# Kernel tuning notes

Hardware: AMD Instinct MI355X
Metric: run time of the kernel (lower is better)

Reference implementation:

```python
import jax, jax.numpy as jnp
import numpy as np

EPS = 1e-5

def _bilinear_sample(xb, ys, xs):
    # xb: [C,H,W]; ys, xs: [H,W] float sample coordinates (zero outside bounds)
    C, H, W = xb.shape
    y0 = jnp.floor(ys); x0 = jnp.floor(xs)
    y1 = y0 + 1.0;      x1 = x0 + 1.0
    wy1 = ys - y0; wy0 = 1.0 - wy1
    wx1 = xs - x0; wx0 = 1.0 - wx1
    def g(yi, xi):
        valid = (yi >= 0) & (yi < H) & (xi >= 0) & (xi < W)
        yc = jnp.clip(yi, 0, H - 1).astype(jnp.int32)
        xc = jnp.clip(xi, 0, W - 1).astype(jnp.int32)
        return xb[:, yc, xc] * valid[None].astype(xb.dtype)  # [C,H,W]
    return (g(y0, x0) * (wy0 * wx0)[None] + g(y0, x1) * (wy0 * wx1)[None]
          + g(y1, x0) * (wy1 * wx0)[None] + g(y1, x1) * (wy1 * wx1)[None])

def _deform_conv2d(x, offset, mask, w, b):
    # x:[B,C,H,W] offset:[B,18,H,W] mask:[B,9,H,W] w:[Co,C,3,3] b:[Co]
    B, C, H, W = x.shape
    Co = w.shape[0]
    ii = jnp.arange(H, dtype=x.dtype)[:, None]
    jj = jnp.arange(W, dtype=x.dtype)[None, :]
    cols = []
    for k in range(9):  # fixed 3x3 kernel positions, row-major (dy=offset[2k], dx=offset[2k+1])
        ky, kx = k // 3 - 1, k % 3 - 1
        ys = ii + ky + offset[:, 2 * k]      # [B,H,W]
        xs = jj + kx + offset[:, 2 * k + 1]
        v = jax.vmap(_bilinear_sample)(x, ys, xs)  # [B,C,H,W]
        cols.append(v * mask[:, k][:, None])
    cols = jnp.stack(cols, axis=1)               # [B,9,C,H,W]
    out = jnp.einsum('bkchw,ock->bohw', cols, w.reshape(Co, C, 9))
    return out + b[None, :, None, None]

def setup_inputs() -> dict:
    key = jax.random.key(0)
    k1, k2, k3, k4 = jax.random.split(key, 4)
    B, Cin, Cout, H, W = 8, 64, 64, 128, 128
    x = jax.random.normal(k1, (B, Cin, H, W), dtype=jnp.float32)
    # offset/mask conv: small weights so learned offsets stay O(1) pixels;
    # bias[18:]=2.0 as in the module's init (masks start near sigmoid(2))
    w_off = jax.random.normal(k2, (27, Cin, 3, 3), dtype=jnp.float32) * 0.01
    b_off = jnp.concatenate([jnp.zeros((18,), jnp.float32), jnp.full((9,), 2.0, jnp.float32)])
    w_dcn = jax.random.normal(k3, (Cout, Cin, 3, 3), dtype=jnp.float32) / np.sqrt(Cin * 9)
    b_dcn = jax.random.normal(k4, (Cout,), dtype=jnp.float32) * 0.01
    return {"x": x, "w_off": w_off, "b_off": b_off, "w_dcn": w_dcn, "b_dcn": b_dcn}

def reference(x, w_off, b_off, w_dcn, b_dcn):
    dn = ('NCHW', 'OIHW', 'NCHW')
    om = jax.lax.conv_general_dilated(x, w_off, (1, 1), 'SAME', dimension_numbers=dn)
    om = om + b_off[None, :, None, None]
    offset = om[:, :18]
    mask = jax.nn.sigmoid(om[:, 18:])
    y = _deform_conv2d(x, offset, mask, w_dcn, b_dcn)
    # InstanceNorm2d (affine=False, biased variance) + ReLU
    mu = jnp.mean(y, axis=(2, 3), keepdims=True)
    var = jnp.var(y, axis=(2, 3), keepdims=True)
    y = (y - mu) * jax.lax.rsqrt(var + EPS)
    return jax.nn.relu(y)
```

## Files before the change

### kernel.cpp

```cpp
#include <hip/hip_runtime.h>
#include <hip/hip_fp16.h>

#define BB   8
#define CIN  64
#define COUT 64
#define HH   128
#define WW   128
#define HWSZ (HH * WW)

typedef _Float16 f16x8 __attribute__((ext_vector_type(8)));
typedef _Float16 h2v   __attribute__((ext_vector_type(2)));
typedef float    f32x4 __attribute__((ext_vector_type(4)));

__device__ __forceinline__ unsigned short f2h_u(float f) {
    __half h = __float2half(f);
    return __half_as_ushort(h);
}
__device__ __forceinline__ float h2f_u(unsigned short u) {
    _Float16 f = *(_Float16*)&u;
    return (float)f;
}
__device__ __forceinline__ unsigned pk2h(float lo, float hi) {
    return (unsigned)f2h_u(lo) | ((unsigned)f2h_u(hi) << 16);
}
__device__ __forceinline__ h2v dupL(unsigned u) { h2v v = *(h2v*)&u; return (h2v){v[0], v[0]}; }
__device__ __forceinline__ h2v dupH(unsigned u) { h2v v = *(h2v*)&u; return (h2v){v[1], v[1]}; }

__device__ __forceinline__ unsigned comb2h(unsigned a, unsigned b, unsigned c, unsigned d,
                                           h2v W0, h2v W1, h2v W2, h2v W3) {
    h2v A = *(h2v*)&a, B = *(h2v*)&b, C = *(h2v*)&c, D = *(h2v*)&d;
    h2v r = A * W0;
    r += B * W1;
    r += C * W2;
    r += D * W3;
    return *(unsigned*)&r;
}


__global__ __launch_bounds__(256) void k_tr(const float* __restrict__ x,
                                            const float* __restrict__ wd,
                                            const float* __restrict__ wof,
                                            unsigned short* __restrict__ xT,
                                            unsigned short* __restrict__ wdT,
                                            unsigned short* __restrict__ wofT,
                                            float4* __restrict__ sums4)
{
    const int t = threadIdx.x;
    const int id = blockIdx.x;
    if (id >= 512) {
        if (id == 512) sums4[t] = make_float4(0.f, 0.f, 0.f, 0.f);
        int base = (id - 512) * 256 + t;
#pragma unroll
        for (int j = 0; j < 4; ++j) {
            int idx = base + j * 16384;
            if (idx < 36864) {
                int k = idx >> 12, rem = idx & 4095, co = rem >> 6, c = rem & 63;
                wdT[idx] = f2h_u(wd[(co * 64 + c) * 9 + k]);
            } else if (idx < 55296) {
                int jj = idx - 36864;
                int k = jj >> 11, rem = jj & 2047, o = rem >> 6, c = rem & 63;
                wofT[jj] = (o < 27) ? f2h_u(wof[(o * 64 + c) * 9 + k]) : 0;
            }
        }
        return;
    }
    __shared__ unsigned short tile[256 * 66];
    const int b = id & 7;
    const int p0 = (id >> 3) * 256;
#pragma unroll
    for (int i = 0; i < 16; ++i) {
        int c = i * 4 + (t >> 6);
        int pl = (t & 63) * 4;
        float4 v = *(const float4*)(x + (((size_t)b * 64 + c) << 14) + p0 + pl);
        tile[(pl + 0) * 66 + c] = f2h_u(v.x);
        tile[(pl + 1) * 66 + c] = f2h_u(v.y);
        tile[(pl + 2) * 66 + c] = f2h_u(v.z);
        tile[(pl + 3) * 66 + c] = f2h_u(v.w);
    }
    __syncthreads();
#pragma unroll
    for (int i = 0; i < 8; ++i) {
        int idd = i * 256 + t;
        int pt = idd >> 3, ck = idd & 7;
        const unsigned* srcp = (const unsigned*)&tile[pt * 66 + ck * 8];
        uint4 r;
        r.x = srcp[0]; r.y = srcp[1]; r.z = srcp[2]; r.w = srcp[3];
        *(uint4*)(xT + ((size_t)b << 20) + ((size_t)(ck >> 2) << 19)
                     + (size_t)(p0 + pt) * 32 + (ck & 3) * 8) = r;
    }
}

__global__ __launch_bounds__(256, 2) void k_off(
    const unsigned short* __restrict__ xT, const unsigned short* __restrict__ wofT,
    const float* __restrict__ bof, unsigned short* __restrict__ om)
{
    __shared__ unsigned short tile[8 * 521 * 8];
    const int t = threadIdx.x;
    const int lane = t & 63, wv = t >> 6;
    const int q = lane >> 4, l15 = lane & 15;
    const int b = blockIdx.x & 7;
    const int xblk = blockIdx.x >> 3;
    const int h0 = xblk * 2;
    const int r0 = h0 - 1;
    const unsigned short* xb = xT + ((size_t)b << 20);

#pragma unroll
    for (int i = 0; i < 17; ++i) {
        int id = i * 256 + t;
        if (id < 4160) {
            int m = id & 7, lin = id >> 3;
            int row = lin / 130, col = lin % 130;
            int gy = r0 + row, gx = col - 1;
            uint4 v = {0u, 0u, 0u, 0u};
            if (((unsigned)gy < (unsigned)HH) && ((unsigned)gx < (unsigned)WW))
                v = *(const uint4*)(xb + ((size_t)(m >> 2) << 19)
                                       + (size_t)(gy * WW + gx) * 32 + (m & 3) * 8);
            *(uint4*)&tile[(m * 521 + lin) * 8] = v;
        }
    }
    __syncthreads();

    const int hrow = h0 + (wv >> 1);
    const int c0 = (wv & 1) * 64;

    f32x4 acc[2][4];
#pragma unroll
    for (int mt = 0; mt < 2; ++mt)
#pragma unroll
        for (int nt = 0; nt < 4; ++nt) acc[mt][nt] = (f32x4){0.f, 0.f, 0.f, 0.f};

#pragma unroll
    for (int k = 0; k < 9; ++k) {
        const int ky = k / 3 - 1, kx = k % 3 - 1;
        const int trow = (hrow - h0) + ky + 1;
        const unsigned short* wk = wofT + k * 2048;
#pragma unroll
        for (int ks = 0; ks < 2; ++ks) {
            f16x8 af[2], bfr[4];
#pragma unroll
            for (int mt = 0; mt < 2; ++mt)
                af[mt] = *(const f16x8*)(wk + (mt * 16 + l15) * 64 + ks * 32 + q * 8);
#pragma unroll
            for (int nt = 0; nt < 4; ++nt) {
                int tc = c0 + nt * 16 + l15 + kx + 1;
                bfr[nt] = *(const f16x8*)&tile[((ks * 4 + q) * 521 + trow * 130 + tc) * 8];
            }
#pragma unroll
            for (int mt = 0; mt < 2; ++mt)
#pragma unroll
                for (int nt = 0; nt < 4; ++nt)
                    acc[mt][nt] = __builtin_amdgcn_mfma_f32_16x16x32_f16(
                        af[mt], bfr[nt], acc[mt][nt], 0, 0, 0);
        }
    }

    const int p0 = xblk * 256 + wv * 64;
    unsigned short* omb = om + (size_t)b * 27 * HWSZ;
#pragma unroll
    for (int mt = 0; mt < 2; ++mt)
#pragma unroll
        for (int r = 0; r < 4; ++r) {
            int o = mt * 16 + q * 4 + r;
            if (o < 27) {
                float bias = bof[o];
#pragma unroll
                for (int nt = 0; nt < 4; ++nt) {
                    int pp = p0 + nt * 16 + l15;
                    float v = acc[mt][nt][r] + bias;
                    if (o >= 18) v = 1.f / (1.f + __expf(-v));
                    omb[(size_t)o * HWSZ + pp] = f2h_u(v);
                }
            }
        }
}

__global__ __launch_bounds__(512, 2) void k_dcn(
    const unsigned short* __restrict__ xT, const unsigned short* __restrict__ om,
    const unsigned short* __restrict__ wdT, const float* __restrict__ bd,
    unsigned short* __restrict__ yh, float2* __restrict__ sums)
{
    __shared__ unsigned short tile_sh[8 * 128 * 32];
    __shared__ uint4          meta_sh[8][64];

    const int t = threadIdx.x;
    const int lane = t & 63, wv = t >> 6;
    const int q = lane >> 4, l15 = lane & 15;
    const int b = blockIdx.x & 7;
    const int pblk = (blockIdx.x >> 3) * 512;
    const int p = pblk + t;
    const int h = p >> 7, w = p & 127;
    const int h0 = pblk >> 7;
    const unsigned short* xbS = xT + ((size_t)b << 20);
    const unsigned short* omp = om + (size_t)b * 27 * HWSZ + p;
    const int gch = q * 8;

    f32x4 acc[4][4];
#pragma unroll
    for (int mt = 0; mt < 4; ++mt)
#pragma unroll
        for (int g = 0; g < 4; ++g) acc[mt][g] = (f32x4){0.f, 0.f, 0.f, 0.f};

#define LOADG2(P, g) { \
    unsigned d0_ = M[g].x; \
    unsigned b0_ = (d0_ & 0x000fffffu) + gch; \
    unsigned sx_ = (d0_ >> 19) & 32u;       \
    unsigned sy_ = (d0_ >> 13) & 4096u;     \
    unsigned b1_ = b0_ + sx_; \
    if (__builtin_expect((int)(d0_ >> 31), 0)) { \
        P[0] = *(const uint4*)(xbh + b0_); \
        P[1] = *(const uint4*)(xbh + b1_); \
        P[2] = *(const uint4*)(xbh + b0_ + sy_); \
        P[3] = *(const uint4*)(xbh + b1_ + sy_); \
    } else { \
        P[0] = *(const uint4*)&tile_sh[b0_]; \
        P[1] = *(const uint4*)&tile_sh[b1_]; \
        P[2] = *(const uint4*)&tile_sh[b0_ + sy_]; \
        P[3] = *(const uint4*)&tile_sh[b1_ + sy_]; \
    } }

#define COMB2(DST, P, g) { \
    h2v W0_ = dupL(M[g].y), W2_ = dupH(M[g].y); \
    h2v W1_ = dupL(M[g].z), W3_ = dupH(M[g].z); \
    uint4 R_; \
    R_.x = comb2h(P[0].x, P[1].x, P[2].x, P[3].x, W0_, W1_, W2_, W3_); \
    R_.y = comb2h(P[0].y, P[1].y, P[2].y, P[3].y, W0_, W1_, W2_, W3_); \
    R_.z = comb2h(P[0].z, P[1].z, P[2].z, P[3].z, W0_, W1_, W2_, W3_); \
    R_.w = comb2h(P[0].w, P[1].w, P[2].w, P[3].w, W0_, W1_, W2_, W3_); \
    DST = *(f16x8*)&R_; }

    for (int hf = 0; hf < 2; ++hf) {
        __syncthreads();
        const unsigned short* xbh = xbS + (hf << 19);
#pragma unroll
        for (int i = 0; i < 8; ++i) {
            int idx = i * 512 + t;
            int s = idx >> 9, u = idx & 511;
            int y = h0 - 2 + s;
            y = min(max(y, 0), HH - 1);
            uint4 v = *(const uint4*)(xbh + (size_t)y * (WW * 32) + u * 8);
            *(uint4*)&tile_sh[idx * 8] = v;
        }
        __syncthreads();

        float offy = h2f_u(omp[0]);
        float offx = h2f_u(omp[HWSZ]);
        float mk   = h2f_u(omp[18 * HWSZ]);

        for (int k = 0; k < 9; ++k) {
            float ys = (float)(h + (k / 3) - 1) + offy;
            float xs = (float)(w + (k % 3) - 1) + offx;
            float fy0 = floorf(ys), fx0 = floorf(xs);
            float wy1 = ys - fy0, wx1 = xs - fx0;
            float wy0 = 1.f - wy1, wx0 = 1.f - wx1;
            int y0 = (int)fy0, x0 = (int)fx0;
            int y1 = y0 + 1, x1 = x0 + 1;
            bool vy0 = (y0 >= 0) && (y0 < HH), vy1 = (y1 >= 0) && (y1 < HH);
            bool vx0 = (x0 >= 0) && (x0 < WW), vx1 = (x1 >= 0) && (x1 < WW);
            int y0c = min(max(y0, 0), HH - 1), y1c = min(max(y1, 0), HH - 1);
            int x0c = min(max(x0, 0), WW - 1), x1c = min(max(x1, 0), WW - 1);
            bool ft = (y0c < h0 - 2) || (y1c > h0 + 5);
            unsigned d0;
            if (!ft) d0 = (unsigned)((y0c - h0 + 2) * 4096 + x0c * 32);
            else     d0 = 0x80000000u | (unsigned)((y0c * WW + x0c) * 32);
            if (x1c != x0c) d0 |= 0x01000000u;
            if (y1c != y0c) d0 |= 0x02000000u;
            float w00 = (vy0 && vx0) ? mk * wy0 * wx0 : 0.f;
            float w01 = (vy0 && vx1) ? mk * wy0 * wx1 : 0.f;
            float w10 = (vy1 && vx0) ? mk * wy1 * wx0 : 0.f;
            float w11 = (vy1 && vx1) ? mk * wy1 * wx1 : 0.f;
            meta_sh[wv][lane] = make_uint4(d0, pk2h(w00, w10), pk2h(w01, w11), 0u);
            int kn = (k < 8) ? k + 1 : 8;
            offy = h2f_u(omp[(2 * kn) * HWSZ]);
            offx = h2f_u(omp[(2 * kn + 1) * HWSZ]);
            mk   = h2f_u(omp[(18 + kn) * HWSZ]);
            __builtin_amdgcn_wave_barrier();

            uint4 M[4];
#pragma unroll
            for (int g = 0; g < 4; ++g)
                M[g] = meta_sh[wv][g * 16 + l15];

            const unsigned short* wk = wdT + k * 4096;
            f16x8 af_[4];
#pragma unroll
            for (int mt = 0; mt < 4; ++mt)
                af_[mt] = *(const f16x8*)(wk + (mt * 16 + l15) * 64 + (hf << 5) + q * 8);

            f16x8 bfr[4];
            uint4 pb[3][4];
            LOADG2(pb[0], 0);
            LOADG2(pb[1], 1);
#pragma unroll
            for (int g = 0; g < 4; ++g) {
                if (g + 2 < 4) LOADG2(pb[(g + 2) % 3], g + 2);
                COMB2(bfr[g], pb[g % 3], g);
            }

#pragma unroll
            for (int mt = 0; mt < 4; ++mt)
#pragma unroll
                for (int g = 0; g < 4; ++g)
                    acc[mt][g] = __builtin_amdgcn_mfma_f32_16x16x32_f16(
                        af_[mt], bfr[g], acc[mt][g], 0, 0, 0);
        }
    }
#undef LOADG2
#undef COMB2

    __syncthreads();
    float* redS = (float*)&meta_sh[0][0];
    float* redQ = redS + 512;
    const int p0 = pblk + wv * 64;
    unsigned short* yb = yh + (size_t)b * COUT * HWSZ;
#pragma unroll
    for (int mt = 0; mt < 4; ++mt)
#pragma unroll
        for (int r = 0; r < 4; ++r) {
            int co = mt * 16 + q * 4 + r;
            float bias = bd[co];
            float s = 0.f, qq = 0.f;
#pragma unroll
            for (int g = 0; g < 4; ++g) {
                float v = acc[mt][g][r] + bias;
                yb[(size_t)co * HWSZ + p0 + g * 16 + l15] = f2h_u(v);
                s += v; qq += v * v;
            }
#pragma unroll
            for (int m = 1; m < 16; m <<= 1) {
                s += __shfl_xor(s, m);
                qq += __shfl_xor(qq, m);
            }
            if (l15 == 0) { redS[wv * 64 + co] = s; redQ[wv * 64 + co] = qq; }
        }
    __syncthreads();
    if (t < 64) {
        float S = 0.f, Q = 0.f;
#pragma unroll
        for (int wvi = 0; wvi < 8; ++wvi) {
            S += redS[wvi * 64 + t];
            Q += redQ[wvi * 64 + t];
        }
        atomicAdd(&sums[b * 64 + t].x, S);
        atomicAdd(&sums[b * 64 + t].y, Q);
    }
}

__global__ __launch_bounds__(256) void k_norm(const unsigned short* __restrict__ yh,
                                              float* __restrict__ out,
                                              const float2* __restrict__ sums)
{
    const int id = blockIdx.x;
    const int b = id & 7;
    const int rest = id >> 3;
    const int co = rest >> 3;
    const int off = rest & 7;
    const int bco = b * 64 + co;
    float2 sq = sums[bco];
    float mu  = sq.x * (1.f / (float)HWSZ);
    float var = sq.y * (1.f / (float)HWSZ) - mu * mu;
    float rstd = rsqrtf(var + 1e-5f);
    const int base = (bco << 14) + off * 2048 + threadIdx.x * 8;
    uint4 v8 = *(const uint4*)(yh + base);
    float4 o0, o1;
    o0.x = fmaxf((h2f_u((unsigned short)(v8.x & 0xffffu)) - mu) * rstd, 0.f);
    o0.y = fmaxf((h2f_u((unsigned short)(v8.x >> 16))     - mu) * rstd, 0.f);
    o0.z = fmaxf((h2f_u((unsigned short)(v8.y & 0xffffu)) - mu) * rstd, 0.f);
    o0.w = fmaxf((h2f_u((unsigned short)(v8.y >> 16))     - mu) * rstd, 0.f);
    o1.x = fmaxf((h2f_u((unsigned short)(v8.z & 0xffffu)) - mu) * rstd, 0.f);
    o1.y = fmaxf((h2f_u((unsigned short)(v8.z >> 16))     - mu) * rstd, 0.f);
    o1.z = fmaxf((h2f_u((unsigned short)(v8.w & 0xffffu)) - mu) * rstd, 0.f);
    o1.w = fmaxf((h2f_u((unsigned short)(v8.w >> 16))     - mu) * rstd, 0.f);
    *(float4*)(out + base)     = o0;
    *(float4*)(out + base + 4) = o1;
}

extern "C" void kernel_launch(void* const* d_in, const int* in_sizes, int n_in,
                              void* d_out, int out_size, void* d_ws, size_t ws_size,
                              hipStream_t stream) {
    const float* x   = (const float*)d_in[0];
    const float* wof = (const float*)d_in[1];
    const float* bof = (const float*)d_in[2];
    const float* wd  = (const float*)d_in[3];
    const float* bd  = (const float*)d_in[4];
    float* out = (float*)d_out;

    char* ws = (char*)d_ws;
    unsigned short* xT   = (unsigned short*)ws;
    unsigned short* om   = (unsigned short*)(ws + 16777216);
    unsigned short* yh   = (unsigned short*)(ws + 23855104);
    unsigned short* wdT  = (unsigned short*)(ws + 40632320);
    unsigned short* wofT = (unsigned short*)(ws + 40706048);
    float2*         sums = (float2*)(ws + 40742912);

    k_tr    <<<576, 256, 0, stream>>>(x, wd, wof, xT, wdT, wofT, (float4*)sums);
    k_off   <<<512, 256, 0, stream>>>(xT, wofT, bof, om);
    k_dcn   <<<256, 512, 0, stream>>>(xT, om, wdT, bd, yh, sums);
    k_norm  <<<4096, 256, 0, stream>>>(yh, out, (const float2*)sums);
}
```

Baseline: 149.6 us.

## Fuse offset/mask convolution into deformable conv kernel via shared-memory staging

Removes the separate offset/mask conv kernel. The fused kernel computes the 27-channel offset/mask conv per block from the same staged x tile that the deformable sampling uses, and keeps the results in LDS instead of writing them to and reading them back from global memory. The half-channel passes are reordered so that the second x half staged for the offset conv is reused directly by the first sampling pass, which saves one restage. The cost is extra LDS per block, since launch_bounds no longer requests 2 blocks per SM, which may reduce occupancy. The per-block offset conv also runs before sampling with no overlap.

Result: faster. 144.4 us, median of 2 (-3.4%).

```diff
diff --git a/kernel.cpp b/kernel.cpp
--- a/kernel.cpp
+++ b/kernel.cpp
@@ -90,96 +90,14 @@
     }
 }
 
-__global__ __launch_bounds__(256, 2) void k_off(
-    const unsigned short* __restrict__ xT, const unsigned short* __restrict__ wofT,
-    const float* __restrict__ bof, unsigned short* __restrict__ om)
-{
-    __shared__ unsigned short tile[8 * 521 * 8];
-    const int t = threadIdx.x;
-    const int lane = t & 63, wv = t >> 6;
-    const int q = lane >> 4, l15 = lane & 15;
-    const int b = blockIdx.x & 7;
-    const int xblk = blockIdx.x >> 3;
-    const int h0 = xblk * 2;
-    const int r0 = h0 - 1;
-    const unsigned short* xb = xT + ((size_t)b << 20);
-
-#pragma unroll
-    for (int i = 0; i < 17; ++i) {
-        int id = i * 256 + t;
-        if (id < 4160) {
-            int m = id & 7, lin = id >> 3;
-            int row = lin / 130, col = lin % 130;
-            int gy = r0 + row, gx = col - 1;
-            uint4 v = {0u, 0u, 0u, 0u};
-            if (((unsigned)gy < (unsigned)HH) && ((unsigned)gx < (unsigned)WW))
-                v = *(const uint4*)(xb + ((size_t)(m >> 2) << 19)
-                                       + (size_t)(gy * WW + gx) * 32 + (m & 3) * 8);
-            *(uint4*)&tile[(m * 521 + lin) * 8] = v;
-        }
-    }
-    __syncthreads();
-
-    const int hrow = h0 + (wv >> 1);
-    const int c0 = (wv & 1) * 64;
-
-    f32x4 acc[2][4];
-#pragma unroll
-    for (int mt = 0; mt < 2; ++mt)
-#pragma unroll
-        for (int nt = 0; nt < 4; ++nt) acc[mt][nt] = (f32x4){0.f, 0.f, 0.f, 0.f};
-
-#pragma unroll
-    for (int k = 0; k < 9; ++k) {
-        const int ky = k / 3 - 1, kx = k % 3 - 1;
-        const int trow = (hrow - h0) + ky + 1;
-        const unsigned short* wk = wofT + k * 2048;
-#pragma unroll
-        for (int ks = 0; ks < 2; ++ks) {
-            f16x8 af[2], bfr[4];
-#pragma unroll
-            for (int mt = 0; mt < 2; ++mt)
-                af[mt] = *(const f16x8*)(wk + (mt * 16 + l15) * 64 + ks * 32 + q * 8);
-#pragma unroll
-            for (int nt = 0; nt < 4; ++nt) {
-                int tc = c0 + nt * 16 + l15 + kx + 1;
-                bfr[nt] = *(const f16x8*)&tile[((ks * 4 + q) * 521 + trow * 130 + tc) * 8];
-            }
-#pragma unroll
-            for (int mt = 0; mt < 2; ++mt)
-#pragma unroll
-                for (int nt = 0; nt < 4; ++nt)
-                    acc[mt][nt] = __builtin_amdgcn_mfma_f32_16x16x32_f16(
-                        af[mt], bfr[nt], acc[mt][nt], 0, 0, 0);
-        }
-    }
-
-    const int p0 = xblk * 256 + wv * 64;
-    unsigned short* omb = om + (size_t)b * 27 * HWSZ;
-#pragma unroll
-    for (int mt = 0; mt < 2; ++mt)
-#pragma unroll
-        for (int r = 0; r < 4; ++r) {
-            int o = mt * 16 + q * 4 + r;
-            if (o < 27) {
-                float bias = bof[o];
-#pragma unroll
-                for (int nt = 0; nt < 4; ++nt) {
-                    int pp = p0 + nt * 16 + l15;
-                    float v = acc[mt][nt][r] + bias;
-                    if (o >= 18) v = 1.f / (1.f + __expf(-v));
-                    omb[(size_t)o * HWSZ + pp] = f2h_u(v);
-                }
-            }
-        }
-}
-
-__global__ __launch_bounds__(512, 2) void k_dcn(
-    const unsigned short* __restrict__ xT, const unsigned short* __restrict__ om,
-    const unsigned short* __restrict__ wdT, const float* __restrict__ bd,
-    unsigned short* __restrict__ yh, float2* __restrict__ sums)
+__global__ __launch_bounds__(512) void k_fused(
+    const unsigned short* __restrict__ xT, const unsigned short* __restrict__ wdT,
+    const unsigned short* __restrict__ wofT, const float* __restrict__ bof,
+    const float* __restrict__ bd, unsigned short* __restrict__ yh,
+    float2* __restrict__ sums)
 {
     __shared__ unsigned short tile_sh[8 * 128 * 32];
+    __shared__ unsigned short om_sh[27 * 512];
     __shared__ uint4          meta_sh[8][64];
 
     const int t = threadIdx.x;
@@ -191,8 +109,82 @@
     const int h = p >> 7, w = p & 127;
     const int h0 = pblk >> 7;
     const unsigned short* xbS = xT + ((size_t)b << 20);
-    const unsigned short* omp = om + (size_t)b * 27 * HWSZ + p;
     const int gch = q * 8;
+
+    const int hrow = h0 + (wv >> 1);
+    const int c0 = (wv & 1) * 64;
+
+#define STAGE(HF) { \
+    const unsigned short* xs_ = xbS + ((HF) << 19); \
+    _Pragma("unroll") \
+    for (int i_ = 0; i_ < 8; ++i_) { \
+        int idx_ = i_ * 512 + t; \
+        int s_ = idx_ >> 9, u_ = idx_ & 511; \
+        int y_ = h0 - 2 + s_; \
+        y_ = min(max(y_, 0), HH - 1); \
+        uint4 v_ = *(const uint4*)(xs_ + (size_t)y_ * (WW * 32) + u_ * 8); \
+        *(uint4*)&tile_sh[idx_ * 8] = v_; \
+    } }
+
+    f32x4 aoff[2][4];
+#pragma unroll
+    for (int mt = 0; mt < 2; ++mt)
+#pragma unroll
+        for (int nt = 0; nt < 4; ++nt) aoff[mt][nt] = (f32x4){0.f, 0.f, 0.f, 0.f};
+
+    for (int hf = 0; hf < 2; ++hf) {
+        __syncthreads();
+        STAGE(hf);
+        __syncthreads();
+#pragma unroll
+        for (int k = 0; k < 9; ++k) {
+            const int ky = k / 3 - 1, kx = k % 3 - 1;
+            if ((unsigned)(hrow + ky) < (unsigned)HH) {
+                const int trow = hrow + ky - (h0 - 2);
+                const unsigned short* wk = wofT + k * 2048;
+                f16x8 af[2];
+#pragma unroll
+                for (int mt = 0; mt < 2; ++mt)
+                    af[mt] = *(const f16x8*)(wk + (mt * 16 + l15) * 64 + hf * 32 + q * 8);
+                f16x8 bfr[4];
+#pragma unroll
+                for (int nt = 0; nt < 4; ++nt) {
+                    int tc = c0 + nt * 16 + l15 + kx;
+                    int tcc = min(max(tc, 0), WW - 1);
+                    f16x8 bv = *(const f16x8*)&tile_sh[trow * 4096 + tcc * 32 + q * 8];
+                    if ((unsigned)tc >= (unsigned)WW)
+                        bv = (f16x8){(_Float16)0, (_Float16)0, (_Float16)0, (_Float16)0,
+                                     (_Float16)0, (_Float16)0, (_Float16)0, (_Float16)0};
+                    bfr[nt] = bv;
+                }
+#pragma unroll
+                for (int mt = 0; mt < 2; ++mt)
+#pragma unroll
+                    for (int nt = 0; nt < 4; ++nt)
+                        aoff[mt][nt] = __builtin_amdgcn_mfma_f32_16x16x32_f16(
+                            af[mt], bfr[nt], aoff[mt][nt], 0, 0, 0);
+            }
+        }
+    }
+    {
+        const int pw = (wv >> 1) * 128 + c0;
+#pragma unroll
+        for (int mt = 0; mt < 2; ++mt)
+#pragma unroll
+            for (int r = 0; r < 4; ++r) {
+                int o = mt * 16 + q * 4 + r;
+                if (o < 27) {
+                    float bias = bof[o];
+#pragma unroll
+                    for (int nt = 0; nt < 4; ++nt) {
+                        float v = aoff[mt][nt][r] + bias;
+                        if (o >= 18) v = 1.f / (1.f + __expf(-v));
+                        om_sh[o * 512 + pw + nt * 16 + l15] = f2h_u(v);
+                    }
+                }
+            }
+    }
+    __syncthreads();
 
     f32x4 acc[4][4];
 #pragma unroll
@@ -228,23 +220,18 @@
     R_.w = comb2h(P[0].w, P[1].w, P[2].w, P[3].w, W0_, W1_, W2_, W3_); \
     DST = *(f16x8*)&R_; }
 
-    for (int hf = 0; hf < 2; ++hf) {
-        __syncthreads();
-        const unsigned short* xbh = xbS + (hf << 19);
-#pragma unroll
-        for (int i = 0; i < 8; ++i) {
-            int idx = i * 512 + t;
-            int s = idx >> 9, u = idx & 511;
-            int y = h0 - 2 + s;
-            y = min(max(y, 0), HH - 1);
-            uint4 v = *(const uint4*)(xbh + (size_t)y * (WW * 32) + u * 8);
-            *(uint4*)&tile_sh[idx * 8] = v;
-        }
-        __syncthreads();
-
-        float offy = h2f_u(omp[0]);
-        float offx = h2f_u(omp[HWSZ]);
-        float mk   = h2f_u(omp[18 * HWSZ]);
+    for (int pass = 0; pass < 2; ++pass) {
+        const int hfg = 1 - pass;
+        if (pass == 1) {
+            __syncthreads();
+            STAGE(0);
+            __syncthreads();
+        }
+        const unsigned short* xbh = xbS + (hfg << 19);
+
+        float offy = h2f_u(om_sh[0 * 512 + t]);
+        float offx = h2f_u(om_sh[1 * 512 + t]);
+        float mk   = h2f_u(om_sh[18 * 512 + t]);
 
         for (int k = 0; k < 9; ++k) {
             float ys = (float)(h + (k / 3) - 1) + offy;
@@ -270,9 +257,9 @@
             float w11 = (vy1 && vx1) ? mk * wy1 * wx1 : 0.f;
             meta_sh[wv][lane] = make_uint4(d0, pk2h(w00, w10), pk2h(w01, w11), 0u);
             int kn = (k < 8) ? k + 1 : 8;
-            offy = h2f_u(omp[(2 * kn) * HWSZ]);
-            offx = h2f_u(omp[(2 * kn + 1) * HWSZ]);
-            mk   = h2f_u(omp[(18 + kn) * HWSZ]);
+            offy = h2f_u(om_sh[(2 * kn) * 512 + t]);
+            offx = h2f_u(om_sh[(2 * kn + 1) * 512 + t]);
+            mk   = h2f_u(om_sh[(18 + kn) * 512 + t]);
             __builtin_amdgcn_wave_barrier();
 
             uint4 M[4];
@@ -284,7 +271,7 @@
             f16x8 af_[4];
 #pragma unroll
             for (int mt = 0; mt < 4; ++mt)
-                af_[mt] = *(const f16x8*)(wk + (mt * 16 + l15) * 64 + (hf << 5) + q * 8);
+                af_[mt] = *(const f16x8*)(wk + (mt * 16 + l15) * 64 + (hfg << 5) + q * 8);
 
             f16x8 bfr[4];
             uint4 pb[3][4];
@@ -306,6 +293,7 @@
     }
 #undef LOADG2
 #undef COMB2
+#undef STAGE
 
     __syncthreads();
     float* redS = (float*)&meta_sh[0][0];
@@ -386,14 +374,12 @@
 
     char* ws = (char*)d_ws;
     unsigned short* xT   = (unsigned short*)ws;
-    unsigned short* om   = (unsigned short*)(ws + 16777216);
-    unsigned short* yh   = (unsigned short*)(ws + 23855104);
-    unsigned short* wdT  = (unsigned short*)(ws + 40632320);
-    unsigned short* wofT = (unsigned short*)(ws + 40706048);
-    float2*         sums = (float2*)(ws + 40742912);
+    unsigned short* yh   = (unsigned short*)(ws + 16777216);
+    unsigned short* wdT  = (unsigned short*)(ws + 33554432);
+    unsigned short* wofT = (unsigned short*)(ws + 33628160);
+    float2*         sums = (float2*)(ws + 33665024);
 
     k_tr    <<<576, 256, 0, stream>>>(x, wd, wof, xT, wdT, wofT, (float4*)sums);
-    k_off   <<<512, 256, 0, stream>>>(xT, wofT, bof, om);
-    k_dcn   <<<256, 512, 0, stream>>>(xT, om, wdT, bd, yh, sums);
+    k_fused <<<256, 512, 0, stream>>>(xT, wdT, wofT, bof, bd, yh, sums);
     k_norm  <<<4096, 256, 0, stream>>>(yh, out, (const float2*)sums);
 }
```
